# Optimization experiments

Measured on AMD Instinct MI355X. Metric: run time of the kernel, lower is better.

## Reference

```python
import jax, jax.numpy as jnp
import numpy as np

N = 10000
D = 128
E = 8192
P_EDGE = 0.002  # avg degree ~20


def setup_inputs() -> dict:
    key = jax.random.key(0)
    ks = jax.random.split(key, 8)
    x = jax.random.normal(ks[0], (N, D), dtype=jnp.float32)
    # binary adjacency matrices (0/1 floats), three different hop/time views
    adj_0_1 = (jax.random.uniform(ks[1], (N, N)) < P_EDGE).astype(jnp.float32)
    adj_1 = (jax.random.uniform(ks[2], (N, N)) < P_EDGE).astype(jnp.float32)
    adj_0_1_2 = (jax.random.uniform(ks[3], (N, N)) < P_EDGE).astype(jnp.float32)
    tar_ei = jax.random.randint(ks[4], (2, E), 0, N, dtype=jnp.int64)
    Wxs = jax.random.normal(ks[5], (4 * D, 1), dtype=jnp.float32) / np.sqrt(4 * D)
    bxs = jnp.zeros((1,), dtype=jnp.float32)
    return {"x": x, "adj_0_1": adj_0_1, "adj_1": adj_1, "adj_0_1_2": adj_0_1_2,
            "tar_ei": tar_ei, "Wxs": Wxs, "bxs": bxs}


def reference(x, adj_0_1, adj_1, adj_0_1_2, tar_ei, Wxs, bxs):
    i, j = tar_ei[0], tar_ei[1]
    xi = x[i]                      # [E, D]
    xj = x[j]                      # [E, D]

    def cn_mask(adj):
        # adjoverlap(adj, adj, tar_ei): common-neighbor indicator per edge, [E, N]
        return adj[i] * adj[j]

    cn_0_1 = cn_mask(adj_0_1)      # [E, N]
    cn_1 = cn_mask(adj_1)
    cn_0_1_2 = cn_mask(adj_0_1_2)
    # sparse set differences
    cn_0 = cn_0_1 * (1.0 - cn_1)
    cn_2 = cn_0_1_2 * (1.0 - cn_0_1)
    # spmm_add: sum node features over each edge's common-neighbor set
    xcn_0 = cn_0 @ x               # [E, D]
    xcn_1 = cn_1 @ x
    xcn_2 = cn_2 @ x

    xij = xi * xj                  # [E, D]
    xs = jnp.concatenate([xij, xcn_0, xcn_1, xcn_2], axis=-1)  # [E, 4D]
    # NOTE: original calls xs.relu() (non in-place) and discards the result -> no-op
    return xs @ Wxs + bxs          # [E, out]
```

## Files before the change

kernel.cpp:

```cpp
#include <hip/hip_runtime.h>
#include <hip/hip_bf16.h>
#include <stdint.h>

typedef unsigned long long u64;

#define N_NODES 10000
#define D_FEAT  128
#define N_EDGES 8192
#define WPR     160
#define WORDS_VALID 157

__device__ __forceinline__ float wave_reduce(float v) {
  #pragma unroll
  for (int o = 32; o > 0; o >>= 1) v += __shfl_xor(v, o, 64);
  return v;
}

__device__ __forceinline__ int tar_stride(const int* tar, int lane) {
  int v = tar[2 * lane + 1];
  return (__ballot(v != 0) == 0ull) ? 2 : 1;
}

__global__ void k_ynode(const float* __restrict__ x, const float* __restrict__ W,
                        float* __restrict__ yn, int* __restrict__ flags) {
  int wid  = (blockIdx.x * blockDim.x + threadIdx.x) >> 6;
  int lane = threadIdx.x & 63;
  if (wid >= N_NODES) return;
  const float* xr = x + (size_t)wid * D_FEAT;
  float x0 = xr[lane], x1 = xr[lane + 64];
  float a0 = x0 * W[128 + lane] + x1 * W[192 + lane];
  float a1 = x0 * W[256 + lane] + x1 * W[320 + lane];
  float a2 = x0 * W[384 + lane] + x1 * W[448 + lane];
  a0 = wave_reduce(a0); a1 = wave_reduce(a1); a2 = wave_reduce(a2);
  if (lane == 0) {
    yn[wid]               = a0;
    yn[N_NODES + wid]     = a1;
    yn[2 * N_NODES + wid] = a2;
    flags[wid] = 0;
  }
}

__global__ void k_setflags(const int* __restrict__ tar, int* __restrict__ flags) {
  int t    = blockIdx.x * blockDim.x + threadIdx.x;
  int lane = threadIdx.x & 63;
  int stride = tar_stride(tar, lane);
  if (t < 2 * N_EDGES) flags[tar[(size_t)t * stride]] = 1;
}

__global__ void k_bitpack(const float* __restrict__ a0m, const float* __restrict__ a1m,
                          const float* __restrict__ a2m, const int* __restrict__ flags,
                          u64* __restrict__ p0, u64* __restrict__ p1, u64* __restrict__ p2) {
  int wg   = (blockIdx.x * blockDim.x + threadIdx.x) >> 6;
  int lane = threadIdx.x & 63;
  if (wg >= 3 * N_NODES) return;
  int mat = wg / N_NODES;
  int row = wg - mat * N_NODES;
  if (!flags[row]) return;
  const float* src = (mat == 0 ? a0m : mat == 1 ? a1m : a2m) + (size_t)row * N_NODES;
  u64* dst = (mat == 0 ? p0 : mat == 1 ? p1 : p2) + (size_t)row * WPR;

  for (int q = 0; q < 39; ++q) {
    int base = q * 256 + lane;
    float f0 = src[base];
    float f1 = src[base + 64];
    float f2 = src[base + 128];
    float f3 = src[base + 192];
    u64 b0 = __ballot(f0 != 0.f);
    u64 b1 = __ballot(f1 != 0.f);
    u64 b2 = __ballot(f2 != 0.f);
    u64 b3 = __ballot(f3 != 0.f);
    if (lane == 0) {
      dst[4 * q]     = b0;
      dst[4 * q + 1] = b1;
      dst[4 * q + 2] = b2;
      dst[4 * q + 3] = b3;
    }
  }
  float ft = (lane < 16) ? src[9984 + lane] : 0.f;
  u64 bt = __ballot(ft != 0.f);
  if (lane == 0) dst[156] = bt;
}

__global__ void k_edge(const float* __restrict__ x, const int* __restrict__ tar,
                       const u64* __restrict__ p0, const u64* __restrict__ p1,
                       const u64* __restrict__ p2, const float* __restrict__ yn,
                       const float* __restrict__ W, const float* __restrict__ b,
                       float* __restrict__ out) {
  int e    = (blockIdx.x * blockDim.x + threadIdx.x) >> 6;
  int lane = threadIdx.x & 63;
  int stride = tar_stride(tar, lane);
  if (e >= N_EDGES) return;
  int i = tar[(size_t)e * stride];
  int j = tar[(size_t)(N_EDGES + e) * stride];

  const float* xi = x + (size_t)i * D_FEAT;
  const float* xj = x + (size_t)j * D_FEAT;
  float acc = xi[lane] * xj[lane] * W[lane] + xi[lane + 64] * xj[lane + 64] * W[lane + 64];

  const u64* r0i = p0 + (size_t)i * WPR; const u64* r0j = p0 + (size_t)j * WPR;
  const u64* r1i = p1 + (size_t)i * WPR; const u64* r1j = p1 + (size_t)j * WPR;
  const u64* r2i = p2 + (size_t)i * WPR; const u64* r2j = p2 + (size_t)j * WPR;
  const float* y0 = yn;
  const float* y1 = yn + N_NODES;
  const float* y2 = yn + 2 * N_NODES;

  for (int w = lane; w < WORDS_VALID; w += 64) {
    u64 m01  = r0i[w] & r0j[w];
    u64 m1   = r1i[w] & r1j[w];
    u64 m012 = r2i[w] & r2j[w];
    u64 m0 = m01  & ~m1;
    u64 m2 = m012 & ~m01;
    int base = w << 6;
    while (m0) { int n = __builtin_ctzll(m0); acc += y0[base + n]; m0 &= m0 - 1; }
    while (m1) { int n = __builtin_ctzll(m1); acc += y1[base + n]; m1 &= m1 - 1; }
    while (m2) { int n = __builtin_ctzll(m2); acc += y2[base + n]; m2 &= m2 - 1; }
  }
  acc = wave_reduce(acc);
  if (lane == 0) out[e] = acc + b[0];
}

__global__ void k_edge_direct(const float* __restrict__ x, const int* __restrict__ tar,
                              const float* __restrict__ a0m, const float* __restrict__ a1m,
                              const float* __restrict__ a2m, const float* __restrict__ W,
                              const float* __restrict__ b, float* __restrict__ out) {
  int e    = (blockIdx.x * blockDim.x + threadIdx.x) >> 6;
  int lane = threadIdx.x & 63;
  int stride = tar_stride(tar, lane);
  if (e >= N_EDGES) return;
  int i = tar[(size_t)e * stride];
  int j = tar[(size_t)(N_EDGES + e) * stride];
  const float* xi = x + (size_t)i * D_FEAT;
  const float* xj = x + (size_t)j * D_FEAT;
  float acc = xi[lane] * xj[lane] * W[lane] + xi[lane + 64] * xj[lane + 64] * W[lane + 64];
  const float* r0i = a0m + (size_t)i * N_NODES; const float* r0j = a0m + (size_t)j * N_NODES;
  const float* r1i = a1m + (size_t)i * N_NODES; const float* r1j = a1m + (size_t)j * N_NODES;
  const float* r2i = a2m + (size_t)i * N_NODES; const float* r2j = a2m + (size_t)j * N_NODES;
  for (int n = lane; n < N_NODES; n += 64) {
    float c01  = r0i[n] * r0j[n];
    float c1   = r1i[n] * r1j[n];
    float c012 = r2i[n] * r2j[n];
    float c0 = c01  * (1.f - c1);
    float c2 = c012 * (1.f - c01);
    if (c0 != 0.f || c1 != 0.f || c2 != 0.f) {
      const float* xn = x + (size_t)n * D_FEAT;
      float s = 0.f;
      for (int d = 0; d < D_FEAT; ++d)
        s += (c0 * W[128 + d] + c1 * W[256 + d] + c2 * W[384 + d]) * xn[d];
      acc += s;
    }
  }
  acc = wave_reduce(acc);
  if (lane == 0) out[e] = acc + b[0];
}

extern "C" void kernel_launch(void* const* d_in, const int* in_sizes, int n_in,
                              void* d_out, int out_size, void* d_ws, size_t ws_size,
                              hipStream_t stream) {
  const float* x    = (const float*)d_in[0];
  const float* a01  = (const float*)d_in[1];
  const float* a1   = (const float*)d_in[2];
  const float* a012 = (const float*)d_in[3];
  const int*   tar  = (const int*)d_in[4];
  const float* W    = (const float*)d_in[5];
  const float* b    = (const float*)d_in[6];
  float* out = (float*)d_out;

  const size_t packed_words = (size_t)N_NODES * WPR;
  const size_t need = 3 * packed_words * sizeof(u64)
                    + 3 * N_NODES * sizeof(float)
                    + N_NODES * sizeof(int);

  if (ws_size >= need) {
    u64* p0 = (u64*)d_ws;
    u64* p1 = p0 + packed_words;
    u64* p2 = p1 + packed_words;
    float* yn  = (float*)(p2 + packed_words);
    int* flags = (int*)(yn + 3 * N_NODES);

    k_ynode   <<<(N_NODES + 3) / 4, 256, 0, stream>>>(x, W, yn, flags);
    k_setflags<<<(2 * N_EDGES + 255) / 256, 256, 0, stream>>>(tar, flags);
    k_bitpack <<<(3 * N_NODES + 3) / 4, 256, 0, stream>>>(a01, a1, a012, flags, p0, p1, p2);
    k_edge    <<<(N_EDGES + 3) / 4, 256, 0, stream>>>(x, tar, p0, p1, p2, yn, W, b, out);
  } else {
    k_edge_direct<<<(N_EDGES + 3) / 4, 256, 0, stream>>>(x, tar, a01, a1, a012, W, b, out);
  }
}
```

Before: 973.1 us.

## Bitpack adjacency rows with float4 loads and strided bit layout, one block per row

The bitpack kernel now gives each adjacency row its own 256-thread block and reads it with float4 loads, so each ballot covers a strided set of columns instead of a contiguous run. The packed word layout changes to match: bit n of word w stands for column 256*(w>>2) + 4n + (w&3). The edge kernel decodes this layout and scans all 160 words. The goal is wider, better-coalesced reads of the bitpack stage, which is bound by reading the large dense adjacency matrices, at the cost of more blocks and a more complex index decode.

Result: no change. 957.5 us (-1.6%).

```diff
diff --git a/kernel.cpp b/kernel.cpp
--- a/kernel.cpp
+++ b/kernel.cpp
@@ -8,7 +8,6 @@
 #define D_FEAT  128
 #define N_EDGES 8192
 #define WPR     160
-#define WORDS_VALID 157
 
 __device__ __forceinline__ float wave_reduce(float v) {
   #pragma unroll
@@ -47,38 +46,44 @@
   if (t < 2 * N_EDGES) flags[tar[(size_t)t * stride]] = 1;
 }
 
-__global__ void k_bitpack(const float* __restrict__ a0m, const float* __restrict__ a1m,
-                          const float* __restrict__ a2m, const int* __restrict__ flags,
-                          u64* __restrict__ p0, u64* __restrict__ p1, u64* __restrict__ p2) {
-  int wg   = (blockIdx.x * blockDim.x + threadIdx.x) >> 6;
-  int lane = threadIdx.x & 63;
-  if (wg >= 3 * N_NODES) return;
-  int mat = wg / N_NODES;
-  int row = wg - mat * N_NODES;
+__global__ __launch_bounds__(256, 8)
+void k_bitpack(const float* __restrict__ a0m, const float* __restrict__ a1m,
+               const float* __restrict__ a2m, const int* __restrict__ flags,
+               u64* __restrict__ p0, u64* __restrict__ p1, u64* __restrict__ p2) {
+  int blk = blockIdx.x;
+  int mat = blk / N_NODES;
+  int row = blk - mat * N_NODES;
   if (!flags[row]) return;
-  const float* src = (mat == 0 ? a0m : mat == 1 ? a1m : a2m) + (size_t)row * N_NODES;
+  int t    = threadIdx.x;
+  int wave = t >> 6;
+  int lane = t & 63;
+  const float4* src4 = reinterpret_cast<const float4*>(
+      (mat == 0 ? a0m : mat == 1 ? a1m : a2m) + (size_t)row * N_NODES);
   u64* dst = (mat == 0 ? p0 : mat == 1 ? p1 : p2) + (size_t)row * WPR;
 
-  for (int q = 0; q < 39; ++q) {
-    int base = q * 256 + lane;
-    float f0 = src[base];
-    float f1 = src[base + 64];
-    float f2 = src[base + 128];
-    float f3 = src[base + 192];
-    u64 b0 = __ballot(f0 != 0.f);
-    u64 b1 = __ballot(f1 != 0.f);
-    u64 b2 = __ballot(f2 != 0.f);
-    u64 b3 = __ballot(f3 != 0.f);
+  #pragma unroll
+  for (int i = 0; i < 5; ++i) {
+    int i0 = 512 * i + t;
+    int i1 = i0 + 256;
+    float4 fa = src4[i0];
+    float4 fb = (i1 < 2500) ? src4[i1] : make_float4(0.f, 0.f, 0.f, 0.f);
+    u64 a0 = __ballot(fa.x != 0.f);
+    u64 a1 = __ballot(fa.y != 0.f);
+    u64 a2 = __ballot(fa.z != 0.f);
+    u64 a3 = __ballot(fa.w != 0.f);
+    u64 b0 = __ballot(fb.x != 0.f);
+    u64 b1 = __ballot(fb.y != 0.f);
+    u64 b2 = __ballot(fb.z != 0.f);
+    u64 b3 = __ballot(fb.w != 0.f);
     if (lane == 0) {
-      dst[4 * q]     = b0;
-      dst[4 * q + 1] = b1;
-      dst[4 * q + 2] = b2;
-      dst[4 * q + 3] = b3;
+      int qa = 8 * i + wave;
+      int qb = qa + 4;
+      u64* da = dst + 4 * qa;
+      u64* db = dst + 4 * qb;
+      da[0] = a0; da[1] = a1; da[2] = a2; da[3] = a3;
+      db[0] = b0; db[1] = b1; db[2] = b2; db[3] = b3;
     }
   }
-  float ft = (lane < 16) ? src[9984 + lane] : 0.f;
-  u64 bt = __ballot(ft != 0.f);
-  if (lane == 0) dst[156] = bt;
 }
 
 __global__ void k_edge(const float* __restrict__ x, const int* __restrict__ tar,
@@ -104,16 +109,17 @@
   const float* y1 = yn + N_NODES;
   const float* y2 = yn + 2 * N_NODES;
 
-  for (int w = lane; w < WORDS_VALID; w += 64) {
+  for (int w = lane; w < WPR; w += 64) {
     u64 m01  = r0i[w] & r0j[w];
     u64 m1   = r1i[w] & r1j[w];
     u64 m012 = r2i[w] & r2j[w];
     u64 m0 = m01  & ~m1;
     u64 m2 = m012 & ~m01;
-    int base = w << 6;
-    while (m0) { int n = __builtin_ctzll(m0); acc += y0[base + n]; m0 &= m0 - 1; }
-    while (m1) { int n = __builtin_ctzll(m1); acc += y1[base + n]; m1 &= m1 - 1; }
-    while (m2) { int n = __builtin_ctzll(m2); acc += y2[base + n]; m2 &= m2 - 1; }
+    int base = (w >> 2) << 8;
+    int c    = w & 3;
+    while (m0) { int n = __builtin_ctzll(m0); acc += y0[base + (n << 2) + c]; m0 &= m0 - 1; }
+    while (m1) { int n = __builtin_ctzll(m1); acc += y1[base + (n << 2) + c]; m1 &= m1 - 1; }
+    while (m2) { int n = __builtin_ctzll(m2); acc += y2[base + (n << 2) + c]; m2 &= m2 - 1; }
   }
   acc = wave_reduce(acc);
   if (lane == 0) out[e] = acc + b[0];
@@ -179,7 +185,7 @@
 
     k_ynode   <<<(N_NODES + 3) / 4, 256, 0, stream>>>(x, W, yn, flags);
     k_setflags<<<(2 * N_EDGES + 255) / 256, 256, 0, stream>>>(tar, flags);
-    k_bitpack <<<(3 * N_NODES + 3) / 4, 256, 0, stream>>>(a01, a1, a012, flags, p0, p1, p2);
+    k_bitpack <<<3 * N_NODES, 256, 0, stream>>>(a01, a1, a012, flags, p0, p1, p2);
     k_edge    <<<(N_EDGES + 3) / 4, 256, 0, stream>>>(x, tar, p0, p1, p2, yn, W, b, out);
   } else {
     k_edge_direct<<<(N_EDGES + 3) / 4, 256, 0, stream>>>(x, tar, a01, a1, a012, W, b, out);
```
